# Kernel optimization log

Measured on AMD Instinct MI355X. Metric: run time of the kernel, lower is better.

The kernel has to match this reference:

```python
import jax, jax.numpy as jnp
import numpy as np

T_THR = 2.0   # temperature for threshold softmax over teachers
T_KD = 20.0   # KD temperature
ALPHA = 0.8   # KD mixing coefficient


def setup_inputs() -> dict:
    key = jax.random.key(0)
    ks = jax.random.split(key, 10)
    B, C = 4096, 1000
    d = {f"outputs{i+1}": jax.random.normal(ks[i], (B, C), dtype=jnp.float32) for i in range(8)}
    d["out_s"] = jax.random.normal(ks[8], (B, C), dtype=jnp.float32)
    d["targets"] = jax.random.randint(ks[9], (B,), 0, C, dtype=jnp.int64)
    return d


def reference(outputs1, outputs2, outputs3, outputs4, outputs5, outputs6, outputs7, outputs8, out_s, targets):
    outs = jnp.stack([outputs1, outputs2, outputs3, outputs4,
                      outputs5, outputs6, outputs7, outputs8])      # [8,B,C]
    mimic = outs.mean(axis=0)                                       # [B,C]
    all9 = jnp.concatenate([outs, mimic[None]], axis=0)             # [9,B,C]

    # per-(teacher,sample) top-2 margin, zero if target is not the argmax
    top2, _ = jax.lax.top_k(all9, 2)                                # [9,B,2]
    tgt_logit = jnp.take_along_axis(all9, targets[None, :, None], axis=2)[..., 0]  # [9,B]
    margin = jnp.where(tgt_logit == top2[..., 0], top2[..., 0] - top2[..., 1], 0.0)  # [9,B]
    thr = jax.nn.softmax(margin / T_THR, axis=0)                    # [9,B] softmax over 9 teachers

    max_preds = outs.max()                                          # scalar over the 8 teachers

    # cross-entropy of student (same for every teacher branch)
    logp_s = jax.nn.log_softmax(out_s, axis=-1)                     # [B,C]
    CE = -jnp.take_along_axis(logp_s, targets[:, None], axis=1)[:, 0]  # [B]

    # KD term per teacher
    logp_sT = jax.nn.log_softmax(out_s / T_KD, axis=-1)             # [B,C]
    p_tT = jax.nn.softmax(all9 / T_KD, axis=-1)                     # [9,B,C]
    KD = -jnp.sum(p_tT * logp_sT[None], axis=-1) * (T_KD * T_KD)    # [9,B]

    # dynamic per-sample weights
    w = tgt_logit / max_preds                                       # [9,B]
    loss = (1.0 - ALPHA * w) * CE[None] + ALPHA * w * KD            # [9,B]

    return jnp.sum(thr * loss, axis=0).mean()
```

## Files before the change

kernel.cpp:

```cpp
#include <hip/hip_runtime.h>

constexpr int   B        = 4096;
constexpr int   C        = 1000;
constexpr float ALPHA    = 0.8f;
constexpr float INV_TKD  = 0.05f;
constexpr float TKD2     = 400.0f;
constexpr float INV_TTHR = 0.5f;
constexpr float SENT     = -1e30f;
constexpr int   NCELL    = 64;

__device__ __forceinline__ unsigned f2ord(float f) {
    unsigned b = __float_as_uint(f);
    return (b & 0x80000000u) ? ~b : (b | 0x80000000u);
}
__device__ __forceinline__ float ord2f(unsigned u) {
    return __uint_as_float((u & 0x80000000u) ? (u & 0x7FFFFFFFu) : ~u);
}

__global__ __launch_bounds__(128) void row_kernel(
    const float* __restrict__ T0, const float* __restrict__ T1,
    const float* __restrict__ T2, const float* __restrict__ T3,
    const float* __restrict__ T4, const float* __restrict__ T5,
    const float* __restrict__ T6, const float* __restrict__ T7,
    const float* __restrict__ S,  const int* __restrict__ TGT,
    double* __restrict__ cell_ce, double* __restrict__ cell_g,
    unsigned* __restrict__ cell_key)
{
    const int tid  = threadIdx.x;
    const int lane = tid & 63;
    const int wid  = tid >> 6;
    const int b    = blockIdx.x;
    const size_t base = (size_t)b * C;
    const bool valid = (tid < 125);

    const int tgt  = TGT[b];
    const int oc8  = tgt >> 3;
    const int slot = tgt & 7;

    __shared__ float4 red[9][2];
    __shared__ float  tvs[9];
    __shared__ float4 sred[2];
    __shared__ float  stv;

    auto load_row = [&](const float* __restrict__ p, float (&v)[8]) {
        if (valid) {
            const float4* p4 = (const float4*)(p + base);
            float4 f0 = p4[2 * tid];
            float4 f1 = p4[2 * tid + 1];
            v[0] = f0.x; v[1] = f0.y; v[2] = f0.z; v[3] = f0.w;
            v[4] = f1.x; v[5] = f1.y; v[6] = f1.z; v[7] = f1.w;
        } else {
#pragma unroll
            for (int i = 0; i < 8; ++i) v[i] = SENT;
        }
    };

    float sv[8];
    load_row(S, sv);
    float va[8], vb[8];
    load_row(T0, va);

    float z1 = 0.0f, zT = 0.0f;
#pragma unroll
    for (int i = 0; i < 8; ++i) {
        z1 += __expf(sv[i]);
        zT += __expf(sv[i] * INV_TKD);
    }
#pragma unroll
    for (int m = 1; m < 64; m <<= 1) {
        z1 += __shfl_xor(z1, m, 64);
        zT += __shfl_xor(zT, m, 64);
    }
    if (lane == 0) sred[wid] = make_float4(z1, zT, 0.0f, 0.0f);
    if (tid == oc8) stv = sv[slot];
    __syncthreads();
    z1 = sred[0].x + sred[1].x;
    zT = sred[0].y + sred[1].y;
    const float logZT = __logf(zT);
    const float ce = __logf(z1) - stv;

    float acc[8];
#pragma unroll
    for (int i = 0; i < 8; ++i) acc[i] = 0.0f;
    float rowmax8 = SENT;
    float mx = 0.0f, s1 = 0.0f, s2 = 0.0f;

    auto process = [&](const float (&w)[8], int br) -> float {
        float m1 = SENT, m2 = SENT;
        float Z = 0.0f, Ss = 0.0f;
#pragma unroll
        for (int i = 0; i < 8; ++i) {
            float x = w[i];
            float n1 = fmaxf(m1, x);
            m2 = fmaxf(fminf(m1, x), m2);
            m1 = n1;
            float e = __expf(x * INV_TKD);
            Z  += e;
            Ss += e * sv[i];
        }
#pragma unroll
        for (int m = 1; m < 64; m <<= 1) {
            float o1 = __shfl_xor(m1, m, 64);
            float o2 = __shfl_xor(m2, m, 64);
            float n1 = fmaxf(m1, o1);
            float n2 = fmaxf(fminf(m1, o1), (m1 >= o1) ? m2 : o2);
            m1 = n1; m2 = n2;
            Z  += __shfl_xor(Z, m, 64);
            Ss += __shfl_xor(Ss, m, 64);
        }
        if (lane == 0) red[br][wid] = make_float4(m1, m2, Z, Ss);
        if (tid == oc8) tvs[br] = w[slot];
        __syncthreads();
        {
            float4 c = red[br][wid];
            float4 o = red[br][wid ^ 1];
            float n1 = fmaxf(c.x, o.x);
            float n2 = fmaxf(fminf(c.x, o.x), (c.x >= o.x) ? c.y : o.y);
            m1 = n1; m2 = n2;
            Z  = c.z + o.z;
            Ss = c.w + o.w;
        }
        const float tval = tvs[br];

        const float kd = TKD2 * (logZT - INV_TKD * (Ss / Z));
        const float margin = (tval == m1) ? (m1 - m2) : 0.0f;
        const float u = tval * (kd - ce);

        const float nmx = fmaxf(mx, margin);
        const float sc  = __expf((mx - nmx) * INV_TTHR);
        const float ee  = __expf((margin - nmx) * INV_TTHR);
        s1 = s1 * sc + ee;
        s2 = s2 * sc + ee * u;
        mx = nmx;
        return m1;
    };

    const float* Tp[8] = {T0, T1, T2, T3, T4, T5, T6, T7};
#pragma unroll
    for (int t = 0; t < 8; t += 2) {
        load_row(Tp[t + 1], vb);
#pragma unroll
        for (int i = 0; i < 8; ++i) acc[i] += va[i];
        rowmax8 = fmaxf(rowmax8, process(va, t));
        if (t + 2 < 8) load_row(Tp[t + 2], va);
#pragma unroll
        for (int i = 0; i < 8; ++i) acc[i] += vb[i];
        rowmax8 = fmaxf(rowmax8, process(vb, t + 1));
    }

#pragma unroll
    for (int i = 0; i < 8; ++i) acc[i] *= 0.125f;
    process(acc, 8);

    if (tid == 0) {
        const int cell = b & (NCELL - 1);
        atomicAdd(cell_ce + cell, (double)ce);
        atomicAdd(cell_g  + cell, (double)(s2 / s1));
        atomicMax(cell_key + cell, f2ord(rowmax8));
    }
}

__global__ __launch_bounds__(64) void fin_kernel(
    const double* __restrict__ cell_ce, const double* __restrict__ cell_g,
    const unsigned* __restrict__ cell_key, float* __restrict__ out)
{
    const int lane = threadIdx.x;
    double ce = cell_ce[lane];
    double g  = cell_g[lane];
    unsigned k = cell_key[lane];
#pragma unroll
    for (int m = 1; m < 64; m <<= 1) {
        ce += __shfl_xor(ce, m, 64);
        g  += __shfl_xor(g, m, 64);
        k   = max(k, (unsigned)__shfl_xor((int)k, m, 64));
    }
    if (lane == 0) {
        const float mp = ord2f(k);
        out[0] = (float)((ce + (double)(ALPHA / mp) * g) * (1.0 / (double)B));
    }
}

extern "C" void kernel_launch(void* const* d_in, const int* in_sizes, int n_in,
                              void* d_out, int out_size, void* d_ws, size_t ws_size,
                              hipStream_t stream)
{
    const float* T0 = (const float*)d_in[0];
    const float* T1 = (const float*)d_in[1];
    const float* T2 = (const float*)d_in[2];
    const float* T3 = (const float*)d_in[3];
    const float* T4 = (const float*)d_in[4];
    const float* T5 = (const float*)d_in[5];
    const float* T6 = (const float*)d_in[6];
    const float* T7 = (const float*)d_in[7];
    const float* S  = (const float*)d_in[8];
    const int*   TG = (const int*)d_in[9];

    double*   cell_ce  = (double*)d_ws;
    double*   cell_g   = cell_ce + NCELL;
    unsigned* cell_key = (unsigned*)(cell_g + NCELL);

    hipMemsetAsync(d_ws, 0, NCELL * (2 * sizeof(double) + sizeof(unsigned)), stream);

    row_kernel<<<B, 128, 0, stream>>>(T0, T1, T2, T3, T4, T5, T6, T7,
                                      S, TG, cell_ce, cell_g, cell_key);
    fin_kernel<<<1, 64, 0, stream>>>(cell_ce, cell_g, cell_key, (float*)d_out);
}
```

Measured before the change: 186.6 us.

## Assign one wavefront per teacher row with shared-memory mimic accumulation

Replaces the 128-thread block that walked all nine teacher branches in sequence with a 576-thread block, one wavefront per teacher plus one for the student. Each teacher wave computes its own top-2, softmax sums and target logit, and adds its row into a shared-memory mimic buffer with atomics. The student wave computes the CE terms and then processes the mimic branch, and thread 0 combines the nine branch results. This exposes more memory-level parallelism per row and removes the serial per-branch block syncs, at the cost of LDS atomics, the student row being reloaded by every wave, and a serialized final branch.

```diff
diff --git a/kernel.cpp b/kernel.cpp
--- a/kernel.cpp
+++ b/kernel.cpp
@@ -17,7 +17,7 @@
     return __uint_as_float((u & 0x80000000u) ? (u & 0x7FFFFFFFu) : ~u);
 }
 
-__global__ __launch_bounds__(128) void row_kernel(
+__global__ __launch_bounds__(576) void row_kernel(
     const float* __restrict__ T0, const float* __restrict__ T1,
     const float* __restrict__ T2, const float* __restrict__ T3,
     const float* __restrict__ T4, const float* __restrict__ T5,
@@ -31,72 +31,54 @@
     const int wid  = tid >> 6;
     const int b    = blockIdx.x;
     const size_t base = (size_t)b * C;
-    const bool valid = (tid < 125);
-
-    const int tgt  = TGT[b];
-    const int oc8  = tgt >> 3;
-    const int slot = tgt & 7;
-
-    __shared__ float4 red[9][2];
-    __shared__ float  tvs[9];
-    __shared__ float4 sred[2];
-    __shared__ float  stv;
-
-    auto load_row = [&](const float* __restrict__ p, float (&v)[8]) {
-        if (valid) {
-            const float4* p4 = (const float4*)(p + base);
-            float4 f0 = p4[2 * tid];
-            float4 f1 = p4[2 * tid + 1];
-            v[0] = f0.x; v[1] = f0.y; v[2] = f0.z; v[3] = f0.w;
-            v[4] = f1.x; v[5] = f1.y; v[6] = f1.z; v[7] = f1.w;
-        } else {
-#pragma unroll
-            for (int i = 0; i < 8; ++i) v[i] = SENT;
+
+    __shared__ float mim[1024];
+    __shared__ float bs_m1[9], bs_m2[9], bs_Z[9], bs_Ss[9], bs_tv[9];
+    __shared__ float s_z1, s_zT, s_stv;
+
+    for (int i = tid; i < 1024; i += 576) mim[i] = 0.0f;
+    __syncthreads();
+
+    const int tgt   = TGT[b];
+    const int uidx  = ((tgt >> 8) << 2) | (tgt & 3);
+    const int slane = (tgt >> 2) & 63;
+
+    const float* rowp = S;
+    if (wid == 0) rowp = T0;  if (wid == 1) rowp = T1;
+    if (wid == 2) rowp = T2;  if (wid == 3) rowp = T3;
+    if (wid == 4) rowp = T4;  if (wid == 5) rowp = T5;
+    if (wid == 6) rowp = T6;  if (wid == 7) rowp = T7;
+
+    auto load_row = [&](const float* __restrict__ p, float (&v)[16]) {
+#pragma unroll
+        for (int k = 0; k < 4; ++k) {
+            if (k < 3 || lane < 58) {
+                float4 f = ((const float4*)(p + base))[lane + 64 * k];
+                v[4*k+0] = f.x; v[4*k+1] = f.y; v[4*k+2] = f.z; v[4*k+3] = f.w;
+            } else {
+                v[4*k+0] = SENT; v[4*k+1] = SENT; v[4*k+2] = SENT; v[4*k+3] = SENT;
+            }
         }
     };
 
-    float sv[8];
-    load_row(S, sv);
-    float va[8], vb[8];
-    load_row(T0, va);
-
-    float z1 = 0.0f, zT = 0.0f;
-#pragma unroll
-    for (int i = 0; i < 8; ++i) {
-        z1 += __expf(sv[i]);
-        zT += __expf(sv[i] * INV_TKD);
-    }
-#pragma unroll
-    for (int m = 1; m < 64; m <<= 1) {
-        z1 += __shfl_xor(z1, m, 64);
-        zT += __shfl_xor(zT, m, 64);
-    }
-    if (lane == 0) sred[wid] = make_float4(z1, zT, 0.0f, 0.0f);
-    if (tid == oc8) stv = sv[slot];
-    __syncthreads();
-    z1 = sred[0].x + sred[1].x;
-    zT = sred[0].y + sred[1].y;
-    const float logZT = __logf(zT);
-    const float ce = __logf(z1) - stv;
-
-    float acc[8];
-#pragma unroll
-    for (int i = 0; i < 8; ++i) acc[i] = 0.0f;
-    float rowmax8 = SENT;
-    float mx = 0.0f, s1 = 0.0f, s2 = 0.0f;
-
-    auto process = [&](const float (&w)[8], int br) -> float {
-        float m1 = SENT, m2 = SENT;
-        float Z = 0.0f, Ss = 0.0f;
-#pragma unroll
-        for (int i = 0; i < 8; ++i) {
+    auto extract = [&](const float (&v)[16]) -> float {
+        float cand = 0.0f;
+#pragma unroll
+        for (int i = 0; i < 16; ++i) cand = (i == uidx) ? v[i] : cand;
+        return __shfl(cand, slane, 64);
+    };
+
+    auto branch = [&](const float (&w)[16], const float (&s)[16], int br) {
+        float m1 = SENT, m2 = SENT, Z = 0.0f, Ss = 0.0f;
+#pragma unroll
+        for (int i = 0; i < 16; ++i) {
             float x = w[i];
             float n1 = fmaxf(m1, x);
             m2 = fmaxf(fminf(m1, x), m2);
             m1 = n1;
             float e = __expf(x * INV_TKD);
             Z  += e;
-            Ss += e * sv[i];
+            Ss += e * s[i];
         }
 #pragma unroll
         for (int m = 1; m < 64; m <<= 1) {
@@ -108,55 +90,85 @@
             Z  += __shfl_xor(Z, m, 64);
             Ss += __shfl_xor(Ss, m, 64);
         }
-        if (lane == 0) red[br][wid] = make_float4(m1, m2, Z, Ss);
-        if (tid == oc8) tvs[br] = w[slot];
-        __syncthreads();
-        {
-            float4 c = red[br][wid];
-            float4 o = red[br][wid ^ 1];
-            float n1 = fmaxf(c.x, o.x);
-            float n2 = fmaxf(fminf(c.x, o.x), (c.x >= o.x) ? c.y : o.y);
-            m1 = n1; m2 = n2;
-            Z  = c.z + o.z;
-            Ss = c.w + o.w;
-        }
-        const float tval = tvs[br];
-
-        const float kd = TKD2 * (logZT - INV_TKD * (Ss / Z));
-        const float margin = (tval == m1) ? (m1 - m2) : 0.0f;
-        const float u = tval * (kd - ce);
-
-        const float nmx = fmaxf(mx, margin);
-        const float sc  = __expf((mx - nmx) * INV_TTHR);
-        const float ee  = __expf((margin - nmx) * INV_TTHR);
-        s1 = s1 * sc + ee;
-        s2 = s2 * sc + ee * u;
-        mx = nmx;
-        return m1;
+        float tv = extract(w);
+        if (lane == 0) {
+            bs_m1[br] = m1; bs_m2[br] = m2;
+            bs_Z[br]  = Z;  bs_Ss[br] = Ss; bs_tv[br] = tv;
+        }
     };
 
-    const float* Tp[8] = {T0, T1, T2, T3, T4, T5, T6, T7};
-#pragma unroll
-    for (int t = 0; t < 8; t += 2) {
-        load_row(Tp[t + 1], vb);
-#pragma unroll
-        for (int i = 0; i < 8; ++i) acc[i] += va[i];
-        rowmax8 = fmaxf(rowmax8, process(va, t));
-        if (t + 2 < 8) load_row(Tp[t + 2], va);
-#pragma unroll
-        for (int i = 0; i < 8; ++i) acc[i] += vb[i];
-        rowmax8 = fmaxf(rowmax8, process(vb, t + 1));
-    }
-
-#pragma unroll
-    for (int i = 0; i < 8; ++i) acc[i] *= 0.125f;
-    process(acc, 8);
+    float v[16];
+    load_row(rowp, v);
+
+    if (wid < 8) {
+        float sv[16];
+        load_row(S, sv);
+
+#pragma unroll
+        for (int k = 0; k < 4; ++k) {
+            if (k < 3 || lane < 58) {
+#pragma unroll
+                for (int j = 0; j < 4; ++j)
+                    atomicAdd(&mim[(4 * k + j) * 64 + lane], v[4*k+j]);
+            }
+        }
+        branch(v, sv, wid);
+    } else {
+        float z1 = 0.0f, zT = 0.0f;
+#pragma unroll
+        for (int i = 0; i < 16; ++i) {
+            z1 += __expf(v[i]);
+            zT += __expf(v[i] * INV_TKD);
+        }
+#pragma unroll
+        for (int m = 1; m < 64; m <<= 1) {
+            z1 += __shfl_xor(z1, m, 64);
+            zT += __shfl_xor(zT, m, 64);
+        }
+        float stv = extract(v);
+        if (lane == 0) { s_z1 = z1; s_zT = zT; s_stv = stv; }
+    }
+    __syncthreads();
+
+    if (wid == 8) {
+        float mv[16];
+#pragma unroll
+        for (int k = 0; k < 4; ++k) {
+            if (k < 3 || lane < 58) {
+#pragma unroll
+                for (int j = 0; j < 4; ++j)
+                    mv[4*k+j] = mim[(4 * k + j) * 64 + lane] * 0.125f;
+            } else {
+                mv[4*k+0] = SENT; mv[4*k+1] = SENT; mv[4*k+2] = SENT; mv[4*k+3] = SENT;
+            }
+        }
+        branch(mv, v, 8);
+    }
+    __syncthreads();
 
     if (tid == 0) {
+        const float ce    = __logf(s_z1) - s_stv;
+        const float logZT = __logf(s_zT);
+        float mx = 0.0f, s1 = 0.0f, s2 = 0.0f, rmax = SENT;
+#pragma unroll
+        for (int br = 0; br < 9; ++br) {
+            const float m1 = bs_m1[br], m2 = bs_m2[br];
+            const float Z  = bs_Z[br],  Ss = bs_Ss[br], tv = bs_tv[br];
+            const float kd = TKD2 * (logZT - INV_TKD * (Ss / Z));
+            const float margin = (tv == m1) ? (m1 - m2) : 0.0f;
+            const float u = tv * (kd - ce);
+            const float nmx = fmaxf(mx, margin);
+            const float sc  = __expf((mx - nmx) * INV_TTHR);
+            const float ee  = __expf((margin - nmx) * INV_TTHR);
+            s1 = s1 * sc + ee;
+            s2 = s2 * sc + ee * u;
+            mx = nmx;
+            if (br < 8) rmax = fmaxf(rmax, m1);
+        }
         const int cell = b & (NCELL - 1);
         atomicAdd(cell_ce + cell, (double)ce);
         atomicAdd(cell_g  + cell, (double)(s2 / s1));
-        atomicMax(cell_key + cell, f2ord(rowmax8));
+        atomicMax(cell_key + cell, f2ord(rmax));
     }
 }
 
@@ -201,7 +213,7 @@
 
     hipMemsetAsync(d_ws, 0, NCELL * (2 * sizeof(double) + sizeof(unsigned)), stream);
 
-    row_kernel<<<B, 128, 0, stream>>>(T0, T1, T2, T3, T4, T5, T6, T7,
+    row_kernel<<<B, 576, 0, stream>>>(T0, T1, T2, T3, T4, T5, T6, T7,
                                       S, TG, cell_ce, cell_g, cell_key);
     fin_kernel<<<1, 64, 0, stream>>>(cell_ce, cell_g, cell_key, (float*)d_out);
 }
```

After: 331.5 us. +77.6%, slower.
